# Performance work log

Hardware: AMD Instinct MI355X
Metric: run time of the kernel (lower is better)

The kernel has to match this reference:

```python
import jax, jax.numpy as jnp
import numpy as np

B, S, E = 2, 2048, 1024
N_HEADS = 16
HEAD_DIM = E // N_HEADS  # 64
ATTN_SCALE = 1.0 / np.sqrt(E)  # NOTE: original scales by 1/sqrt(hidden_dim_phi), not head_dim
ROPE_BASE = 10000.0


def _rope(t):
    # t: (B, H, S, D) with D = HEAD_DIM; interleaved-pair RoPE (torchtune-style)
    d = t.shape[-1]
    s = t.shape[-2]
    inv_freq = 1.0 / (ROPE_BASE ** (jnp.arange(0, d, 2, dtype=jnp.float32) / d))  # (D/2,)
    ang = jnp.arange(s, dtype=jnp.float32)[:, None] * inv_freq[None, :]  # (S, D/2)
    cos, sin = jnp.cos(ang), jnp.sin(ang)  # (S, D/2)
    tp = t.reshape(t.shape[:-1] + (d // 2, 2))
    te, to = tp[..., 0], tp[..., 1]  # (B,H,S,D/2)
    oe = te * cos - to * sin
    oo = te * sin + to * cos
    return jnp.stack([oe, oo], axis=-1).reshape(t.shape)


def setup_inputs() -> dict:
    key = jax.random.key(0)
    ks = jax.random.split(key, 5)
    std = 0.02
    return {
        "x": jax.random.normal(ks[0], (B, S, E), dtype=jnp.float32),
        "W_q": jax.random.normal(ks[1], (E, E), dtype=jnp.float32) * std,
        "W_k": jax.random.normal(ks[2], (E, E), dtype=jnp.float32) * std,
        "W_v": jax.random.normal(ks[3], (E, E), dtype=jnp.float32) * std,
        "W_o": jax.random.normal(ks[4], (E, E), dtype=jnp.float32) * std,
    }


def reference(x, W_q, W_k, W_v, W_o):
    b, s, e = x.shape
    hd = e // N_HEADS
    # projections -> (B, H, S, D)
    def proj(w):
        return (x @ w).reshape(b, s, N_HEADS, hd).transpose(0, 2, 1, 3)
    q = _rope(proj(W_q))
    k = _rope(proj(W_k))
    v = proj(W_v)
    scores = jnp.einsum('bhsd,bhtd->bhst', q, k) * ATTN_SCALE  # (B,H,S,S)
    causal = jnp.triu(jnp.ones((s, s), dtype=bool), k=1)
    scores = jnp.where(causal, -jnp.inf, scores)
    probs = jax.nn.softmax(scores, axis=-1)  # dropout is identity in eval mode
    out = jnp.einsum('bhst,bhtd->bhsd', probs, v)
    out = out.transpose(0, 2, 1, 3).reshape(b, s, e)
    return out @ W_o
```

## Files before the change

kernel.cpp:

```cpp
#include <hip/hip_runtime.h>
#include <hip/hip_bf16.h>

#define S_LEN 2048
#define E_DIM 1024
#define NH 16
#define HD 64
#define ATTN_SCALE 0.03125f
#define KVB 128

typedef __attribute__((ext_vector_type(8))) short short8;
typedef __attribute__((ext_vector_type(8))) unsigned short ushort8;
typedef __attribute__((ext_vector_type(4))) unsigned short ushort4_t;
typedef __attribute__((ext_vector_type(4))) float f32x4;
typedef __attribute__((ext_vector_type(4))) float f4;

__device__ __forceinline__ float bf2f(unsigned short u) {
    unsigned int x = ((unsigned int)u) << 16;
    return __builtin_bit_cast(float, x);
}
__device__ __forceinline__ unsigned short f2bf(float f) {
    unsigned int x = __builtin_bit_cast(unsigned int, f);
    x += 0x7FFFu + ((x >> 16) & 1u);
    return (unsigned short)(x >> 16);
}
__device__ __forceinline__ void gload16(const unsigned short* g, unsigned short* l) {
    __builtin_amdgcn_global_load_lds(
        (__attribute__((address_space(1))) void*)g,
        (__attribute__((address_space(3))) void*)l, 16, 0, 0);
}

__global__ __launch_bounds__(256) void k_convert(const float* __restrict__ x,
                                                 unsigned short* __restrict__ xb) {
    size_t i = ((size_t)blockIdx.x * 256 + threadIdx.x) * 8;
    f4 a = *(const f4*)(x + i);
    f4 b = *(const f4*)(x + i + 4);
    ushort8 o;
    o[0] = f2bf(a[0]); o[1] = f2bf(a[1]); o[2] = f2bf(a[2]); o[3] = f2bf(a[3]);
    o[4] = f2bf(b[0]); o[5] = f2bf(b[1]); o[6] = f2bf(b[2]); o[7] = f2bf(b[3]);
    *(ushort8*)(xb + i) = o;
}

__global__ __launch_bounds__(256) void k_transw(const float* W0, const float* W1,
                                                const float* W2, const float* W3,
                                                unsigned short* T0, unsigned short* T1,
                                                unsigned short* T2, unsigned short* T3) {
    const float* W; unsigned short* T;
    switch (blockIdx.z) {
        case 0: W = W0; T = T0; break;
        case 1: W = W1; T = T1; break;
        case 2: W = W2; T = T2; break;
        default: W = W3; T = T3; break;
    }
    __shared__ float tile[32][33];
    int tx = threadIdx.x, ty = threadIdx.y;
    int bx = blockIdx.x * 32, by = blockIdx.y * 32;
#pragma unroll
    for (int i = 0; i < 4; i++)
        tile[ty + i * 8][tx] = W[(size_t)(by + ty + i * 8) * E_DIM + bx + tx];
    __syncthreads();
#pragma unroll
    for (int i = 0; i < 4; i++)
        T[(size_t)(bx + ty + i * 8) * E_DIM + by + tx] = f2bf(tile[tx][ty + i * 8]);
}

__global__ __launch_bounds__(256) void k_rope_table(float* __restrict__ cosT,
                                                    float* __restrict__ sinT) {
    int idx = blockIdx.x * 256 + threadIdx.x;
    int s = idx >> 5, j = idx & 31;
    float inv = expf(-(float)j * (9.210340371976184f / 32.f));
    float ang = (float)s * inv;
    cosT[idx] = cosf(ang);
    sinT[idx] = sinf(ang);
}

template <int BM, int BN, int WGM, int WGN, int NBN, bool QKV3>
__global__ __launch_bounds__(WGM * WGN * 64, 2)
void k_gemm2(const unsigned short* __restrict__ A,
             const unsigned short* __restrict__ B,
             unsigned short* __restrict__ Qo,
             unsigned short* __restrict__ Ko,
             unsigned short* __restrict__ Vto,
             float* __restrict__ Fo,
             const float* __restrict__ cosT,
             const float* __restrict__ sinT) {
    constexpr int THREADS = WGM * WGN * 64;
    constexpr int WM = BM / WGM, WN = BN / WGN;
    constexpr int FM = WM / 16, FN = WN / 16;
    constexpr int NT = E_DIM / 64;
    constexpr int AR = BM * 8 / THREADS;
    constexpr int BR = BN * 8 / THREADS;
    constexpr int STG = AR + BR;
    constexpr int MB = 4096 / BM;
    constexpr int NWG = MB * NBN;
    __shared__ unsigned short Al[2][BM * 64];
    __shared__ unsigned short Bl[2][BN * 64];
    int tid = threadIdx.x, lane = tid & 63, wid = tid >> 6;
    int l15 = lane & 15, lg = lane >> 4;
    int wr = wid / WGN, wc = wid % WGN;
    int orig = blockIdx.y * NBN + blockIdx.x;
    int wg = (orig & 7) * (NWG / 8) + (orig >> 3);
    int bm = wg / NBN, bn = wg % NBN;

    auto stage = [&](int buf, int k0) {
#pragma unroll
        for (int i = 0; i < AR; i++) {
            int r = i * (THREADS / 8) + wid * 8 + (lane >> 3);
            int cs = (lane & 7) ^ (r & 7);
            gload16(A + (size_t)(bm * BM + r) * E_DIM + k0 + cs * 8,
                    &Al[buf][i * (THREADS * 8) + wid * 512]);
        }
#pragma unroll
        for (int i = 0; i < BR; i++) {
            int r = i * (THREADS / 8) + wid * 8 + (lane >> 3);
            int cs = (lane & 7) ^ (r & 7);
            gload16(B + (size_t)(bn * BN + r) * E_DIM + k0 + cs * 8,
                    &Bl[buf][i * (THREADS * 8) + wid * 512]);
        }
    };

    f32x4 acc[FM][FN] = {};
    stage(0, 0);
    for (int t = 0; t < NT; t++) {
        int cur = t & 1;
        if (t + 1 < NT) {
            stage(cur ^ 1, (t + 1) * 64);
            asm volatile("s_waitcnt vmcnt(%0)" :: "n"(STG) : "memory");
        } else {
            asm volatile("s_waitcnt vmcnt(0)" ::: "memory");
        }
        __builtin_amdgcn_s_barrier();
        __builtin_amdgcn_sched_barrier(0);
#pragma unroll
        for (int ks = 0; ks < 2; ks++) {
            short8 af[FM], bfv[FN];
#pragma unroll
            for (int m = 0; m < FM; m++) {
                int r = wr * WM + m * 16 + l15;
                int gc = ks * 4 + lg;
                af[m] = *(const short8*)&Al[cur][r * 64 + ((gc ^ (r & 7)) << 3)];
            }
#pragma unroll
            for (int n = 0; n < FN; n++) {
                int r = wc * WN + n * 16 + l15;
                int gc = ks * 4 + lg;
                bfv[n] = *(const short8*)&Bl[cur][r * 64 + ((gc ^ (r & 7)) << 3)];
            }
#pragma unroll
            for (int m = 0; m < FM; m++)
#pragma unroll
                for (int n = 0; n < FN; n++)
                    acc[m][n] = __builtin_amdgcn_mfma_f32_16x16x32_bf16(
                        af[m], bfv[n], acc[m][n], 0, 0, 0);
        }
        __builtin_amdgcn_s_barrier();
    }
#pragma unroll
    for (int m = 0; m < FM; m++) {
        int r0 = bm * BM + wr * WM + m * 16 + lg * 4;
#pragma unroll
        for (int n = 0; n < FN; n++) {
            int colg = bn * BN + wc * WN + n * 16 + l15;
            if (QKV3) {
                int z = colg >> 10, c1 = colg & 1023;
                if (z == 2) {
                    int h = c1 >> 6, d = c1 & 63;
                    int bb = r0 >> 11, s = r0 & 2047;
                    ushort4_t p;
#pragma unroll
                    for (int r = 0; r < 4; r++) p[r] = f2bf(acc[m][n][r]);
                    *(ushort4_t*)(Vto + (((size_t)((bb * 16 + h) * 64 + d)) << 11) + s) = p;
                } else {
                    unsigned short* T = z ? Ko : Qo;
                    int dl = c1 & 63, j = dl >> 1;
                    float sgn = (dl & 1) ? 1.f : -1.f;
                    float sc = z ? 1.f : ATTN_SCALE;
#pragma unroll
                    for (int r = 0; r < 4; r++) {
                        int row = r0 + r, s = row & 2047;
                        float c = cosT[s * 32 + j], sn = sinT[s * 32 + j];
                        float v = acc[m][n][r];
                        float p = __shfl_xor(v, 1);
                        T[(size_t)row * E_DIM + c1] = f2bf((v * c + sgn * p * sn) * sc);
                    }
                }
            } else {
#pragma unroll
                for (int r = 0; r < 4; r++)
                    Fo[(size_t)(r0 + r) * E_DIM + colg] = acc[m][n][r];
            }
        }
    }
}

__global__ __launch_bounds__(256, 2) void k_attn(const unsigned short* __restrict__ Q,
                                                 const unsigned short* __restrict__ K,
                                                 const unsigned short* __restrict__ Vt,
                                                 unsigned short* __restrict__ O) {
    __shared__ unsigned short K_lds[128 * 64];
    __shared__ unsigned short V_lds[64 * 128];
    __shared__ unsigned short P_lds[4][16][136];
    int tid = threadIdx.x, lane = tid & 63, wid = tid >> 6;
    int l15 = lane & 15, lg = lane >> 4;
    int orig = blockIdx.y * 16 + blockIdx.x;
    int wg = (orig & 7) * 64 + (orig >> 3);
    int jp = wg & 15, bh = wg >> 4;
    int b = bh >> 4, h = bh & 15;
    const size_t base_qk = (size_t)b * S_LEN * E_DIM + (size_t)h * HD;
    const unsigned short* Vbh = Vt + ((size_t)(bh * 64) << 11);

    auto stageK = [&](int kt) {
        const unsigned short* Kb = K + base_qk + (size_t)(kt * KVB) * E_DIM;
#pragma unroll
        for (int i = 0; i < 4; i++) {
            int r = i * 32 + wid * 8 + (lane >> 3);
            int cs = (lane & 7) ^ (r & 7);
            gload16(Kb + (size_t)r * E_DIM + cs * 8, K_lds + i * 2048 + wid * 512);
        }
    };
    auto stageV = [&](int kt) {
#pragma unroll
        for (int i = 0; i < 4; i++) {
            int r = i * 16 + wid * 4 + (lane >> 4);
            int cs = (lane & 15) ^ (r & 7);
            gload16(Vbh + (size_t)r * 2048 + kt * KVB + cs * 8,
                    V_lds + i * 2048 + wid * 512);
        }
    };

    for (int pass = 0; pass < 2; ++pass) {
        int qt = pass ? (31 - jp) : jp;
        const unsigned short* Qb = Q + base_qk + (size_t)(qt * 64 + wid * 16) * E_DIM;
        short8 bq[2];
#pragma unroll
        for (int s2 = 0; s2 < 2; s2++)
            bq[s2] = *(const short8*)(Qb + (size_t)l15 * E_DIM + s2 * 32 + lg * 8);
        f32x4 acc_o[4] = {};
        float m_i = -1e30f, l_i = 0.f;
        int q_glob = qt * 64 + wid * 16 + l15;
        int nkt = (qt + 2) >> 1;
        stageK(0);
        stageV(0);
        asm volatile("s_waitcnt vmcnt(4)" ::: "memory");
        __builtin_amdgcn_s_barrier();
        __builtin_amdgcn_sched_barrier(0);
        for (int kt = 0; kt < nkt; ++kt) {
            f32x4 acc_s[8] = {};
            __builtin_amdgcn_s_setprio(1);
#pragma unroll
            for (int mf = 0; mf < 8; mf++) {
                int rK = mf * 16 + l15;
#pragma unroll
                for (int s2 = 0; s2 < 2; s2++) {
                    int gc = s2 * 4 + lg;
                    short8 a = *(const short8*)&K_lds[rK * 64 + ((gc ^ (rK & 7)) << 3)];
                    acc_s[mf] = __builtin_amdgcn_mfma_f32_16x16x32_bf16(
                        a, bq[s2], acc_s[mf], 0, 0, 0);
                }
            }
            __builtin_amdgcn_s_setprio(0);
            __builtin_amdgcn_s_barrier();
            if (kt + 1 < nkt) stageK(kt + 1);
            float sv[32];
            float vmax = -1e30f;
            if (kt == nkt - 1) {
#pragma unroll
                for (int mf = 0; mf < 8; mf++)
#pragma unroll
                    for (int r = 0; r < 4; r++) {
                        int kg = kt * KVB + mf * 16 + lg * 4 + r;
                        float v = acc_s[mf][r];
                        if (kg > q_glob) v = -1e30f;
                        sv[mf * 4 + r] = v;
                        vmax = fmaxf(vmax, v);
                    }
            } else {
#pragma unroll
                for (int mf = 0; mf < 8; mf++)
#pragma unroll
                    for (int r = 0; r < 4; r++) {
                        float v = acc_s[mf][r];
                        sv[mf * 4 + r] = v;
                        vmax = fmaxf(vmax, v);
                    }
            }
            vmax = fmaxf(vmax, __shfl_xor(vmax, 16));
            vmax = fmaxf(vmax, __shfl_xor(vmax, 32));
            float m_new = fmaxf(m_i, vmax);
            float corr = __expf(m_i - m_new);
            float rowsum = 0.f;
#pragma unroll
            for (int i = 0; i < 32; i++) {
                float p = __expf(sv[i] - m_new);
                sv[i] = p;
                rowsum += p;
            }
            rowsum += __shfl_xor(rowsum, 16);
            rowsum += __shfl_xor(rowsum, 32);
            l_i = l_i * corr + rowsum;
            m_i = m_new;
#pragma unroll
            for (int mf = 0; mf < 8; mf++) {
                ushort4_t pk;
#pragma unroll
                for (int r = 0; r < 4; r++) pk[r] = f2bf(sv[mf * 4 + r]);
                *(ushort4_t*)&P_lds[wid][l15][mf * 16 + lg * 4] = pk;
            }
#pragma unroll
            for (int r = 0; r < 4; r++) {
                float c4 = __shfl(corr, lg * 4 + r);
#pragma unroll
                for (int nf = 0; nf < 4; nf++) acc_o[nf][r] *= c4;
            }
            if (kt + 1 < nkt)
                asm volatile("s_waitcnt vmcnt(4)" ::: "memory");
            else
                asm volatile("s_waitcnt vmcnt(0)" ::: "memory");
            __builtin_amdgcn_s_barrier();
            __builtin_amdgcn_sched_barrier(0);
            __builtin_amdgcn_s_setprio(1);
#pragma unroll
            for (int s2 = 0; s2 < 4; s2++) {
                short8 pa = *(const short8*)&P_lds[wid][l15][s2 * 32 + lg * 8];
#pragma unroll
                for (int nf = 0; nf < 4; nf++) {
                    int rV = nf * 16 + l15;
                    int gc = s2 * 4 + lg;
                    short8 bv = *(const short8*)&V_lds[rV * 128 + ((gc ^ (rV & 7)) << 3)];
                    acc_o[nf] = __builtin_amdgcn_mfma_f32_16x16x32_bf16(
                        pa, bv, acc_o[nf], 0, 0, 0);
                }
            }
            __builtin_amdgcn_s_setprio(0);
            __builtin_amdgcn_s_barrier();
            if (kt + 1 < nkt) {
                stageV(kt + 1);
                asm volatile("s_waitcnt vmcnt(4)" ::: "memory");
            }
            __builtin_amdgcn_s_barrier();
            __builtin_amdgcn_sched_barrier(0);
        }
        unsigned short* Ob = O + base_qk + (size_t)(qt * 64 + wid * 16) * E_DIM;
#pragma unroll
        for (int r = 0; r < 4; r++) {
            float linv = 1.f / __shfl(l_i, lg * 4 + r);
#pragma unroll
            for (int nf = 0; nf < 4; nf++)
                Ob[(size_t)(lg * 4 + r) * E_DIM + nf * 16 + l15] =
                    f2bf(acc_o[nf][r] * linv);
        }
    }
}

extern "C" void kernel_launch(void* const* d_in, const int* in_sizes, int n_in,
                              void* d_out, int out_size, void* d_ws, size_t ws_size,
                              hipStream_t stream) {
    (void)in_sizes; (void)n_in; (void)out_size; (void)ws_size;
    const float* x  = (const float*)d_in[0];
    const float* Wq = (const float*)d_in[1];
    const float* Wk = (const float*)d_in[2];
    const float* Wv = (const float*)d_in[3];
    const float* Wo = (const float*)d_in[4];

    unsigned short* us = (unsigned short*)d_ws;
    unsigned short* xb    = us;
    unsigned short* WqkvT = us + 4194304;
    unsigned short* WoT   = us + 7340032;
    unsigned short* Qb    = us + 8388608;
    unsigned short* Kb    = us + 12582912;
    unsigned short* Vt    = us + 16777216;
    unsigned short* AO    = us + 20971520;
    float* cosT = (float*)((char*)d_ws + 50331648);
    float* sinT = cosT + 65536;

    k_convert<<<2048, 256, 0, stream>>>(x, xb);
    k_transw<<<dim3(32, 32, 4), dim3(32, 8), 0, stream>>>(
        Wq, Wk, Wv, Wo, WqkvT, WqkvT + 1048576, WqkvT + 2097152, WoT);
    k_rope_table<<<256, 256, 0, stream>>>(cosT, sinT);
    k_gemm2<128, 128, 2, 2, 24, true><<<dim3(24, 32), 256, 0, stream>>>(
        xb, WqkvT, Qb, Kb, Vt, nullptr, cosT, sinT);
    k_attn<<<dim3(16, 32), 256, 0, stream>>>(Qb, Kb, Vt, AO);
    k_gemm2<128, 64, 2, 2, 16, false><<<dim3(16, 32), 256, 0, stream>>>(
        AO, WoT, nullptr, nullptr, nullptr, (float*)d_out, cosT, sinT);
}
```

Measured before the change: 115.0 us.

## Triple-buffer GEMM K-loop with BK=32, raise MFMA priority, retile projections

Replaces the double-buffered BK=64 GEMM mainloop with a three-stage ring of BK=32 LDS buffers. Global loads now run two stages ahead, with hand-set vmcnt waits, and the XOR swizzle is adapted to 4-chunk rows. MFMA sections are wrapped in s_setprio to favour compute waves. The QKV projection moves to 256x256 tiles with 512 threads, which leaves only 192 workgroups and large LDS use per block, so the GPU may be under-filled. The output projection moves to 128x128 tiles.

```diff
diff --git a/kernel.cpp b/kernel.cpp
--- a/kernel.cpp
+++ b/kernel.cpp
@@ -75,7 +75,7 @@
 
 template <int BM, int BN, int WGM, int WGN, int NBN, bool QKV3>
 __global__ __launch_bounds__(WGM * WGN * 64, 2)
-void k_gemm2(const unsigned short* __restrict__ A,
+void k_gemm3(const unsigned short* __restrict__ A,
              const unsigned short* __restrict__ B,
              unsigned short* __restrict__ Qo,
              unsigned short* __restrict__ Ko,
@@ -86,14 +86,13 @@
     constexpr int THREADS = WGM * WGN * 64;
     constexpr int WM = BM / WGM, WN = BN / WGN;
     constexpr int FM = WM / 16, FN = WN / 16;
-    constexpr int NT = E_DIM / 64;
-    constexpr int AR = BM * 8 / THREADS;
-    constexpr int BR = BN * 8 / THREADS;
-    constexpr int STG = AR + BR;
+    constexpr int NT = E_DIM / 32;
+    constexpr int RA = BM * 4 / THREADS;
+    constexpr int RB = BN * 4 / THREADS;
     constexpr int MB = 4096 / BM;
     constexpr int NWG = MB * NBN;
-    __shared__ unsigned short Al[2][BM * 64];
-    __shared__ unsigned short Bl[2][BN * 64];
+    __shared__ unsigned short Al[3][BM * 32];
+    __shared__ unsigned short Bl[3][BN * 32];
     int tid = threadIdx.x, lane = tid & 63, wid = tid >> 6;
     int l15 = lane & 15, lg = lane >> 4;
     int wr = wid / WGN, wc = wid % WGN;
@@ -101,57 +100,59 @@
     int wg = (orig & 7) * (NWG / 8) + (orig >> 3);
     int bm = wg / NBN, bn = wg % NBN;
 
-    auto stage = [&](int buf, int k0) {
-#pragma unroll
-        for (int i = 0; i < AR; i++) {
-            int r = i * (THREADS / 8) + wid * 8 + (lane >> 3);
-            int cs = (lane & 7) ^ (r & 7);
+    auto stage = [&](int t) {
+        int buf = t % 3;
+        int k0 = t * 32;
+#pragma unroll
+        for (int i = 0; i < RA; i++) {
+            int r = i * (THREADS / 4) + wid * 16 + (lane >> 2);
+            int cs = (lane & 3) ^ (r & 3);
             gload16(A + (size_t)(bm * BM + r) * E_DIM + k0 + cs * 8,
                     &Al[buf][i * (THREADS * 8) + wid * 512]);
         }
 #pragma unroll
-        for (int i = 0; i < BR; i++) {
-            int r = i * (THREADS / 8) + wid * 8 + (lane >> 3);
-            int cs = (lane & 7) ^ (r & 7);
+        for (int i = 0; i < RB; i++) {
+            int r = i * (THREADS / 4) + wid * 16 + (lane >> 2);
+            int cs = (lane & 3) ^ (r & 3);
             gload16(B + (size_t)(bn * BN + r) * E_DIM + k0 + cs * 8,
                     &Bl[buf][i * (THREADS * 8) + wid * 512]);
         }
     };
 
     f32x4 acc[FM][FN] = {};
-    stage(0, 0);
+    stage(0);
+    stage(1);
     for (int t = 0; t < NT; t++) {
-        int cur = t & 1;
-        if (t + 1 < NT) {
-            stage(cur ^ 1, (t + 1) * 64);
-            asm volatile("s_waitcnt vmcnt(%0)" :: "n"(STG) : "memory");
+        int cur = t % 3;
+        if (t + 2 < NT) {
+            stage(t + 2);
+            asm volatile("s_waitcnt vmcnt(8)" ::: "memory");
+        } else if (t + 1 < NT) {
+            asm volatile("s_waitcnt vmcnt(4)" ::: "memory");
         } else {
             asm volatile("s_waitcnt vmcnt(0)" ::: "memory");
         }
         __builtin_amdgcn_s_barrier();
         __builtin_amdgcn_sched_barrier(0);
-#pragma unroll
-        for (int ks = 0; ks < 2; ks++) {
-            short8 af[FM], bfv[FN];
-#pragma unroll
-            for (int m = 0; m < FM; m++) {
-                int r = wr * WM + m * 16 + l15;
-                int gc = ks * 4 + lg;
-                af[m] = *(const short8*)&Al[cur][r * 64 + ((gc ^ (r & 7)) << 3)];
-            }
-#pragma unroll
-            for (int n = 0; n < FN; n++) {
-                int r = wc * WN + n * 16 + l15;
-                int gc = ks * 4 + lg;
-                bfv[n] = *(const short8*)&Bl[cur][r * 64 + ((gc ^ (r & 7)) << 3)];
-            }
-#pragma unroll
-            for (int m = 0; m < FM; m++)
-#pragma unroll
-                for (int n = 0; n < FN; n++)
-                    acc[m][n] = __builtin_amdgcn_mfma_f32_16x16x32_bf16(
-                        af[m], bfv[n], acc[m][n], 0, 0, 0);
-        }
+        short8 af[FM], bfv[FN];
+#pragma unroll
+        for (int m = 0; m < FM; m++) {
+            int r = wr * WM + m * 16 + l15;
+            af[m] = *(const short8*)&Al[cur][r * 32 + ((lg ^ (r & 3)) << 3)];
+        }
+#pragma unroll
+        for (int n = 0; n < FN; n++) {
+            int r = wc * WN + n * 16 + l15;
+            bfv[n] = *(const short8*)&Bl[cur][r * 32 + ((lg ^ (r & 3)) << 3)];
+        }
+        __builtin_amdgcn_s_setprio(1);
+#pragma unroll
+        for (int m = 0; m < FM; m++)
+#pragma unroll
+            for (int n = 0; n < FN; n++)
+                acc[m][n] = __builtin_amdgcn_mfma_f32_16x16x32_bf16(
+                    af[m], bfv[n], acc[m][n], 0, 0, 0);
+        __builtin_amdgcn_s_setprio(0);
         __builtin_amdgcn_s_barrier();
     }
 #pragma unroll
@@ -376,9 +377,9 @@
     k_transw<<<dim3(32, 32, 4), dim3(32, 8), 0, stream>>>(
         Wq, Wk, Wv, Wo, WqkvT, WqkvT + 1048576, WqkvT + 2097152, WoT);
     k_rope_table<<<256, 256, 0, stream>>>(cosT, sinT);
-    k_gemm2<128, 128, 2, 2, 24, true><<<dim3(24, 32), 256, 0, stream>>>(
+    k_gemm3<256, 256, 2, 4, 12, true><<<dim3(12, 16), 512, 0, stream>>>(
         xb, WqkvT, Qb, Kb, Vt, nullptr, cosT, sinT);
     k_attn<<<dim3(16, 32), 256, 0, stream>>>(Qb, Kb, Vt, AO);
-    k_gemm2<128, 64, 2, 2, 16, false><<<dim3(16, 32), 256, 0, stream>>>(
+    k_gemm3<128, 128, 2, 2, 8, false><<<dim3(8, 32), 256, 0, stream>>>(
         AO, WoT, nullptr, nullptr, nullptr, (float*)d_out, cosT, sinT);
 }
```

Measured after the change: 132.7 us. +15.4%, slower.

## Replace QKV projection GEMM with 256x256 8-wave ping-pong pipelined kernel

Applied to the files above, without the earlier changes.

The fused QKV projection moves to a new kernel with 256x256 tiles and 512 threads (8 waves). Each K-step is split into four quarter-tile MFMA phases, and loads of the next A/B halves are interleaved with compute using explicit waitcnt, barriers and raised s_setprio. The goal is more operand reuse per LDS byte and overlap of global loads with MFMA work. The cost is a much smaller grid (192 blocks) that may not fill all CUs, plus fragile hand-placed synchronization. The output projection GEMM is split off into its own simplified template.

```diff
diff --git a/kernel.cpp b/kernel.cpp
--- a/kernel.cpp
+++ b/kernel.cpp
@@ -73,16 +73,161 @@
     sinT[idx] = sinf(ang);
 }
 
-template <int BM, int BN, int WGM, int WGN, int NBN, bool QKV3>
-__global__ __launch_bounds__(WGM * WGN * 64, 2)
-void k_gemm2(const unsigned short* __restrict__ A,
+__global__ __launch_bounds__(512, 2)
+void k_gemm8(const unsigned short* __restrict__ A,
              const unsigned short* __restrict__ B,
              unsigned short* __restrict__ Qo,
              unsigned short* __restrict__ Ko,
              unsigned short* __restrict__ Vto,
-             float* __restrict__ Fo,
              const float* __restrict__ cosT,
              const float* __restrict__ sinT) {
+    constexpr int NT = 16;
+    constexpr int NBN = 12;
+    __shared__ unsigned short Al[2][2][8192];
+    __shared__ unsigned short Bl[2][2][8192];
+    int tid = threadIdx.x, lane = tid & 63, wid = tid >> 6;
+    int l15 = lane & 15, lg = lane >> 4;
+    int wr = wid >> 2, wc = wid & 3;
+    int orig = blockIdx.y * NBN + blockIdx.x;
+    int wg = (orig & 7) * 24 + (orig >> 3);
+    int bm = wg / NBN, bn = wg % NBN;
+    int sr = tid >> 3, sc = tid & 7;
+    const unsigned short* Abase = A + (size_t)(bm * 256) * E_DIM;
+    const unsigned short* Bbase = B + (size_t)(bn * 256) * E_DIM;
+
+    auto stageA = [&](int buf, int half, int kt) {
+#pragma unroll
+        for (int i = 0; i < 2; i++) {
+            int r = i * 64 + sr;
+            int cs = sc ^ (r & 7);
+            gload16(Abase + (size_t)(half * 128 + r) * E_DIM + kt * 64 + cs * 8,
+                    &Al[buf][half][i * 4096 + tid * 8]);
+        }
+    };
+    auto stageB = [&](int buf, int half, int kt) {
+#pragma unroll
+        for (int i = 0; i < 2; i++) {
+            int r = i * 64 + sr;
+            int cs = sc ^ (r & 7);
+            gload16(Bbase + (size_t)(half * 128 + r) * E_DIM + kt * 64 + cs * 8,
+                    &Bl[buf][half][i * 4096 + tid * 8]);
+        }
+    };
+
+    f32x4 acc[8][4] = {};
+    short8 af[8], bf0[4], bf1[4];
+    int swz = l15 & 7;
+
+    auto ldsA = [&](int cur, int mh) {
+#pragma unroll
+        for (int j = 0; j < 4; j++)
+#pragma unroll
+            for (int ks = 0; ks < 2; ks++)
+                af[j * 2 + ks] = *(const short8*)
+                    &Al[cur][wr][(mh * 64 + j * 16 + l15) * 64 +
+                                 (((ks * 4 + lg) ^ swz) << 3)];
+    };
+    auto ldsB = [&](int cur, int nh, short8* bf) {
+#pragma unroll
+        for (int n = 0; n < 2; n++)
+#pragma unroll
+            for (int ks = 0; ks < 2; ks++)
+                bf[n * 2 + ks] = *(const short8*)
+                    &Bl[cur][wc >> 1][((wc & 1) * 64 + (nh * 2 + n) * 16 + l15) * 64 +
+                                      (((ks * 4 + lg) ^ swz) << 3)];
+    };
+    auto mma = [&](int mh, int nh, short8* bf) {
+        __builtin_amdgcn_s_setprio(1);
+#pragma unroll
+        for (int j = 0; j < 4; j++)
+#pragma unroll
+            for (int n = 0; n < 2; n++)
+#pragma unroll
+                for (int ks = 0; ks < 2; ks++)
+                    acc[mh * 4 + j][nh * 2 + n] = __builtin_amdgcn_mfma_f32_16x16x32_bf16(
+                        af[j * 2 + ks], bf[n * 2 + ks], acc[mh * 4 + j][nh * 2 + n], 0, 0, 0);
+        __builtin_amdgcn_s_setprio(0);
+    };
+
+    stageA(0, 0, 0); stageA(0, 1, 0);
+    stageB(0, 0, 0); stageB(0, 1, 0);
+    stageB(1, 0, 1); stageB(1, 1, 1);
+    asm volatile("s_waitcnt vmcnt(4)" ::: "memory");
+    __builtin_amdgcn_s_barrier();
+    __builtin_amdgcn_sched_barrier(0);
+
+    for (int kt = 0; kt < NT; kt++) {
+        int cur = kt & 1;
+        int ka = kt + 1 < NT ? kt + 1 : NT - 1;
+        int kb = kt + 2 < NT ? kt + 2 : NT - 1;
+        ldsA(cur, 0);
+        ldsB(cur, 0, bf0);
+        stageA(cur ^ 1, 0, ka);
+        asm volatile("s_waitcnt lgkmcnt(8)" ::: "memory");
+        __builtin_amdgcn_s_barrier();
+        asm volatile("s_waitcnt lgkmcnt(0)" ::: "memory");
+        __builtin_amdgcn_sched_barrier(0);
+        mma(0, 0, bf0);
+        __builtin_amdgcn_s_barrier();
+        ldsB(cur, 1, bf1);
+        stageA(cur ^ 1, 1, ka);
+        __builtin_amdgcn_s_barrier();
+        asm volatile("s_waitcnt lgkmcnt(0)" ::: "memory");
+        __builtin_amdgcn_sched_barrier(0);
+        mma(0, 1, bf1);
+        __builtin_amdgcn_s_barrier();
+        ldsA(cur, 1);
+        stageB(cur, 0, kb);
+        __builtin_amdgcn_s_barrier();
+        asm volatile("s_waitcnt lgkmcnt(0)" ::: "memory");
+        __builtin_amdgcn_sched_barrier(0);
+        mma(1, 1, bf1);
+        __builtin_amdgcn_s_barrier();
+        stageB(cur, 1, kb);
+        asm volatile("s_waitcnt vmcnt(4)" ::: "memory");
+        __builtin_amdgcn_s_barrier();
+        __builtin_amdgcn_sched_barrier(0);
+        mma(1, 0, bf0);
+        __builtin_amdgcn_s_barrier();
+    }
+
+#pragma unroll
+    for (int m = 0; m < 8; m++) {
+        int r0 = bm * 256 + wr * 128 + m * 16 + lg * 4;
+#pragma unroll
+        for (int n = 0; n < 4; n++) {
+            int colg = bn * 256 + wc * 64 + n * 16 + l15;
+            int z = colg >> 10, c1 = colg & 1023;
+            if (z == 2) {
+                int h = c1 >> 6, d = c1 & 63;
+                int bb = r0 >> 11, s = r0 & 2047;
+                ushort4_t p;
+#pragma unroll
+                for (int r = 0; r < 4; r++) p[r] = f2bf(acc[m][n][r]);
+                *(ushort4_t*)(Vto + (((size_t)((bb * 16 + h) * 64 + d)) << 11) + s) = p;
+            } else {
+                unsigned short* T = z ? Ko : Qo;
+                int dl = c1 & 63, j = dl >> 1;
+                float sgn = (dl & 1) ? 1.f : -1.f;
+                float scq = z ? 1.f : ATTN_SCALE;
+#pragma unroll
+                for (int r = 0; r < 4; r++) {
+                    int row = r0 + r, s = row & 2047;
+                    float c = cosT[s * 32 + j], sn = sinT[s * 32 + j];
+                    float v = acc[m][n][r];
+                    float p = __shfl_xor(v, 1);
+                    T[(size_t)row * E_DIM + c1] = f2bf((v * c + sgn * p * sn) * scq);
+                }
+            }
+        }
+    }
+}
+
+template <int BM, int BN, int WGM, int WGN, int NBN>
+__global__ __launch_bounds__(WGM * WGN * 64, 2)
+void k_gemmo(const unsigned short* __restrict__ A,
+             const unsigned short* __restrict__ B,
+             float* __restrict__ Fo) {
     constexpr int THREADS = WGM * WGN * 64;
     constexpr int WM = BM / WGM, WN = BN / WGN;
     constexpr int FM = WM / 16, FN = WN / 16;
@@ -90,8 +235,7 @@
     constexpr int AR = BM * 8 / THREADS;
     constexpr int BR = BN * 8 / THREADS;
     constexpr int STG = AR + BR;
-    constexpr int MB = 4096 / BM;
-    constexpr int NWG = MB * NBN;
+    constexpr int NWG = (4096 / BM) * NBN;
     __shared__ unsigned short Al[2][BM * 64];
     __shared__ unsigned short Bl[2][BN * 64];
     int tid = threadIdx.x, lane = tid & 63, wid = tid >> 6;
@@ -160,34 +304,9 @@
 #pragma unroll
         for (int n = 0; n < FN; n++) {
             int colg = bn * BN + wc * WN + n * 16 + l15;
-            if (QKV3) {
-                int z = colg >> 10, c1 = colg & 1023;
-                if (z == 2) {
-                    int h = c1 >> 6, d = c1 & 63;
-                    int bb = r0 >> 11, s = r0 & 2047;
-                    ushort4_t p;
-#pragma unroll
-                    for (int r = 0; r < 4; r++) p[r] = f2bf(acc[m][n][r]);
-                    *(ushort4_t*)(Vto + (((size_t)((bb * 16 + h) * 64 + d)) << 11) + s) = p;
-                } else {
-                    unsigned short* T = z ? Ko : Qo;
-                    int dl = c1 & 63, j = dl >> 1;
-                    float sgn = (dl & 1) ? 1.f : -1.f;
-                    float sc = z ? 1.f : ATTN_SCALE;
-#pragma unroll
-                    for (int r = 0; r < 4; r++) {
-                        int row = r0 + r, s = row & 2047;
-                        float c = cosT[s * 32 + j], sn = sinT[s * 32 + j];
-                        float v = acc[m][n][r];
-                        float p = __shfl_xor(v, 1);
-                        T[(size_t)row * E_DIM + c1] = f2bf((v * c + sgn * p * sn) * sc);
-                    }
-                }
-            } else {
-#pragma unroll
-                for (int r = 0; r < 4; r++)
-                    Fo[(size_t)(r0 + r) * E_DIM + colg] = acc[m][n][r];
-            }
+#pragma unroll
+            for (int r = 0; r < 4; r++)
+                Fo[(size_t)(r0 + r) * E_DIM + colg] = acc[m][n][r];
         }
     }
 }
@@ -376,9 +495,8 @@
     k_transw<<<dim3(32, 32, 4), dim3(32, 8), 0, stream>>>(
         Wq, Wk, Wv, Wo, WqkvT, WqkvT + 1048576, WqkvT + 2097152, WoT);
     k_rope_table<<<256, 256, 0, stream>>>(cosT, sinT);
-    k_gemm2<128, 128, 2, 2, 24, true><<<dim3(24, 32), 256, 0, stream>>>(
-        xb, WqkvT, Qb, Kb, Vt, nullptr, cosT, sinT);
+    k_gemm8<<<dim3(12, 16), 512, 0, stream>>>(xb, WqkvT, Qb, Kb, Vt, cosT, sinT);
     k_attn<<<dim3(16, 32), 256, 0, stream>>>(Qb, Kb, Vt, AO);
-    k_gemm2<128, 64, 2, 2, 16, false><<<dim3(16, 32), 256, 0, stream>>>(
-        AO, WoT, nullptr, nullptr, nullptr, (float*)d_out, cosT, sinT);
-}
+    k_gemmo<128, 64, 2, 2, 16><<<dim3(16, 32), 256, 0, stream>>>(
+        AO, WoT, (float*)d_out);
+}
```

Result: slower. 118.0 us (+2.6%).
